# Kernel optimization log

Hardware: AMD Instinct MI355X
Metric: run time of the kernel (lower is better)

Reference implementation:

```python
import jax, jax.numpy as jnp
import numpy as np

N, D_IN, D_OUT = 500000, 128, 128
DROP_P = 0.5


def setup_inputs() -> dict:
    key = jax.random.key(0)
    k1, k2, k3, k4 = jax.random.split(key, 4)
    x = jax.random.normal(k1, (N, D_IN), dtype=jnp.float32)
    weight = jax.random.normal(k2, (D_IN, D_OUT), dtype=jnp.float32)
    support = jax.random.normal(k3, (D_OUT, D_OUT), dtype=jnp.float32)
    # inverted-dropout mask: Bernoulli(keep=1-p) scaled by 1/(1-p), matching F.dropout in training mode
    keep = 1.0 - DROP_P
    u = jax.random.uniform(k4, (N, D_IN), dtype=jnp.float32)
    drop_mask = (u < keep).astype(jnp.float32) / keep
    return {"x": x, "weight": weight, "support": support, "drop_mask": drop_mask}


def reference(x, weight, support, drop_mask):
    # training-mode dropout (deterministic mask), dense transform, right-multiply by support, ReLU
    xd = x * drop_mask                      # [N, D_IN]
    xw = jnp.matmul(xd, weight)             # [N, D_OUT]
    out = jnp.matmul(xw, support)           # [N, D_OUT]
    return jax.nn.relu(out)
```

## Files before the change

kernel.cpp:

```cpp
#include <hip/hip_runtime.h>
#include <hip/hip_bf16.h>


#define D 128

typedef __attribute__((ext_vector_type(8))) short short8;
typedef __attribute__((ext_vector_type(4))) float f32x4;

__device__ __forceinline__ short f2bf(float f) {
    union { __hip_bfloat16 h; short s; } u;
    u.h = __float2bfloat16(f);
    return u.s;
}

__global__ void wprod_kernel(const float* __restrict__ weight,
                             const float* __restrict__ support,
                             unsigned short* __restrict__ wt) {
    __shared__ float wrow[D];
    const int i = blockIdx.x;
    const int j = threadIdx.x;
    wrow[j] = weight[i * D + j];
    __syncthreads();
    float acc = 0.f;
#pragma unroll 8
    for (int k = 0; k < D; ++k)
        acc = fmaf(wrow[k], support[k * D + j], acc);
    union { __hip_bfloat16 h; unsigned short s; } u;
    u.h = __float2bfloat16(acc);
    wt[(size_t)j * D + i] = u.s;
}

__global__ __launch_bounds__(256, 4) void gcn_fused(
    const float* __restrict__ x, const float* __restrict__ mask,
    const unsigned short* __restrict__ wt, float* __restrict__ out,
    int nslabs) {
    __shared__ __align__(16) unsigned short lw[D * D];

    const uint4* src = reinterpret_cast<const uint4*>(wt);
    for (int c = threadIdx.x; c < 2048; c += 256) {
        const int n = c >> 4;
        const int gs = (c & 15) ^ (n & 7);
        *reinterpret_cast<uint4*>(&lw[(n << 7) + (gs << 3)]) = src[c];
    }
    __syncthreads();

    const int lane = threadIdx.x & 63;
    const int m = lane & 15;
    const int quad = lane >> 4;
    const int mx = m & 7;

    const int wave = (int)((blockIdx.x * blockDim.x + threadIdx.x) >> 6);
    const int nwaves = (int)((gridDim.x * blockDim.x) >> 6);

    const int rowoff = m * D + quad * 8;

    int s = wave;
    if (s >= nslabs) return;

    f32x4 vx[8], vm[8];

    {
        const float* xr = x + (size_t)s * (16 * D) + rowoff;
        const float* mr = mask + (size_t)s * (16 * D) + rowoff;
#pragma unroll
        for (int kk = 0; kk < 4; ++kk) {
            vx[2 * kk]     = *reinterpret_cast<const f32x4*>(xr + kk * 32);
            vx[2 * kk + 1] = *reinterpret_cast<const f32x4*>(xr + kk * 32 + 4);
            vm[2 * kk]     = *reinterpret_cast<const f32x4*>(mr + kk * 32);
            vm[2 * kk + 1] = *reinterpret_cast<const f32x4*>(mr + kk * 32 + 4);
        }
    }

    while (true) {
        short8 a[4];
#pragma unroll
        for (int kk = 0; kk < 4; ++kk) {
            f32x4 p0 = vx[2 * kk] * vm[2 * kk];
            f32x4 p1 = vx[2 * kk + 1] * vm[2 * kk + 1];
            short8 v;
            v[0] = f2bf(p0[0]); v[1] = f2bf(p0[1]);
            v[2] = f2bf(p0[2]); v[3] = f2bf(p0[3]);
            v[4] = f2bf(p1[0]); v[5] = f2bf(p1[1]);
            v[6] = f2bf(p1[2]); v[7] = f2bf(p1[3]);
            a[kk] = v;
        }

        const int snext = s + nwaves;
        const bool more = snext < nslabs;
        if (more) {
            const float* xr = x + (size_t)snext * (16 * D) + rowoff;
            const float* mr = mask + (size_t)snext * (16 * D) + rowoff;
#pragma unroll
            for (int kk = 0; kk < 4; ++kk) {
                vx[2 * kk]     = *reinterpret_cast<const f32x4*>(xr + kk * 32);
                vx[2 * kk + 1] = *reinterpret_cast<const f32x4*>(xr + kk * 32 + 4);
                vm[2 * kk]     = *reinterpret_cast<const f32x4*>(mr + kk * 32);
                vm[2 * kk + 1] = *reinterpret_cast<const f32x4*>(mr + kk * 32 + 4);
            }
        }

        float* orow = out + (size_t)s * (16 * D) + m * D;
#pragma unroll
        for (int n = 0; n < 8; ++n) {
            f32x4 acc = {0.f, 0.f, 0.f, 0.f};
#pragma unroll
            for (int kk = 0; kk < 4; ++kk) {
                const short8 b = *reinterpret_cast<const short8*>(
                    &lw[(((n << 4) + m) << 7) + ((((kk << 2) + quad) ^ mx) << 3)]);
                acc = __builtin_amdgcn_mfma_f32_16x16x32_bf16(b, a[kk], acc, 0, 0, 0);
            }
            f32x4 rv;
#pragma unroll
            for (int r = 0; r < 4; ++r) rv[r] = acc[r] > 0.f ? acc[r] : 0.f;
            *reinterpret_cast<f32x4*>(&orow[(n << 4) + (quad << 2)]) = rv;
        }

        if (!more) break;
        s = snext;
    }
}

extern "C" void kernel_launch(void* const* d_in, const int* in_sizes, int n_in,
                              void* d_out, int out_size, void* d_ws, size_t ws_size,
                              hipStream_t stream) {
    const float* x = (const float*)d_in[0];
    const float* weight = (const float*)d_in[1];
    const float* support = (const float*)d_in[2];
    const float* mask = (const float*)d_in[3];
    float* out = (float*)d_out;
    unsigned short* wt = (unsigned short*)d_ws;

    const int nrows = in_sizes[0] / D;
    const int nslabs = nrows / 16;

    wprod_kernel<<<dim3(D), dim3(D), 0, stream>>>(weight, support, wt);
    gcn_fused<<<dim3(1024), dim3(256), 0, stream>>>(x, mask, wt, out, nslabs);
}
```

Measured before the change: 772.1 us.

## Drop register prefetch, use nontemporal loads, double block size for occupancy

```diff
diff --git a/kernel.cpp b/kernel.cpp
--- a/kernel.cpp
+++ b/kernel.cpp
@@ -30,14 +30,14 @@
     wt[(size_t)j * D + i] = u.s;
 }
 
-__global__ __launch_bounds__(256, 4) void gcn_fused(
+__global__ __launch_bounds__(512, 8) void gcn_fused(
     const float* __restrict__ x, const float* __restrict__ mask,
     const unsigned short* __restrict__ wt, float* __restrict__ out,
     int nslabs) {
     __shared__ __align__(16) unsigned short lw[D * D];
 
     const uint4* src = reinterpret_cast<const uint4*>(wt);
-    for (int c = threadIdx.x; c < 2048; c += 256) {
+    for (int c = threadIdx.x; c < 2048; c += 512) {
         const int n = c >> 4;
         const int gs = (c & 15) ^ (n & 7);
         *reinterpret_cast<uint4*>(&lw[(n << 7) + (gs << 3)]) = src[c];
@@ -54,49 +54,29 @@
 
     const int rowoff = m * D + quad * 8;
 
-    int s = wave;
-    if (s >= nslabs) return;
-
-    f32x4 vx[8], vm[8];
-
-    {
+    for (int s = wave; s < nslabs; s += nwaves) {
         const float* xr = x + (size_t)s * (16 * D) + rowoff;
         const float* mr = mask + (size_t)s * (16 * D) + rowoff;
-#pragma unroll
-        for (int kk = 0; kk < 4; ++kk) {
-            vx[2 * kk]     = *reinterpret_cast<const f32x4*>(xr + kk * 32);
-            vx[2 * kk + 1] = *reinterpret_cast<const f32x4*>(xr + kk * 32 + 4);
-            vm[2 * kk]     = *reinterpret_cast<const f32x4*>(mr + kk * 32);
-            vm[2 * kk + 1] = *reinterpret_cast<const f32x4*>(mr + kk * 32 + 4);
-        }
-    }
 
-    while (true) {
         short8 a[4];
 #pragma unroll
         for (int kk = 0; kk < 4; ++kk) {
-            f32x4 p0 = vx[2 * kk] * vm[2 * kk];
-            f32x4 p1 = vx[2 * kk + 1] * vm[2 * kk + 1];
+            f32x4 x0 = __builtin_nontemporal_load(
+                reinterpret_cast<const f32x4*>(xr + kk * 32));
+            f32x4 x1 = __builtin_nontemporal_load(
+                reinterpret_cast<const f32x4*>(xr + kk * 32 + 4));
+            f32x4 m0 = __builtin_nontemporal_load(
+                reinterpret_cast<const f32x4*>(mr + kk * 32));
+            f32x4 m1 = __builtin_nontemporal_load(
+                reinterpret_cast<const f32x4*>(mr + kk * 32 + 4));
+            f32x4 p0 = x0 * m0;
+            f32x4 p1 = x1 * m1;
             short8 v;
             v[0] = f2bf(p0[0]); v[1] = f2bf(p0[1]);
             v[2] = f2bf(p0[2]); v[3] = f2bf(p0[3]);
             v[4] = f2bf(p1[0]); v[5] = f2bf(p1[1]);
             v[6] = f2bf(p1[2]); v[7] = f2bf(p1[3]);
             a[kk] = v;
-        }
-
-        const int snext = s + nwaves;
-        const bool more = snext < nslabs;
-        if (more) {
-            const float* xr = x + (size_t)snext * (16 * D) + rowoff;
-            const float* mr = mask + (size_t)snext * (16 * D) + rowoff;
-#pragma unroll
-            for (int kk = 0; kk < 4; ++kk) {
-                vx[2 * kk]     = *reinterpret_cast<const f32x4*>(xr + kk * 32);
-                vx[2 * kk + 1] = *reinterpret_cast<const f32x4*>(xr + kk * 32 + 4);
-                vm[2 * kk]     = *reinterpret_cast<const f32x4*>(mr + kk * 32);
-                vm[2 * kk + 1] = *reinterpret_cast<const f32x4*>(mr + kk * 32 + 4);
-            }
         }
 
         float* orow = out + (size_t)s * (16 * D) + m * D;
@@ -114,9 +94,6 @@
             for (int r = 0; r < 4; ++r) rv[r] = acc[r] > 0.f ? acc[r] : 0.f;
             *reinterpret_cast<f32x4*>(&orow[(n << 4) + (quad << 2)]) = rv;
         }
-
-        if (!more) break;
-        s = snext;
     }
 }
 
@@ -134,5 +111,5 @@
     const int nslabs = nrows / 16;
 
     wprod_kernel<<<dim3(D), dim3(D), 0, stream>>>(weight, support, wt);
-    gcn_fused<<<dim3(1024), dim3(256), 0, stream>>>(x, mask, wt, out, nslabs);
+    gcn_fused<<<dim3(1024), dim3(512), 0, stream>>>(x, mask, wt, out, nslabs);
 }
```

Result: no change. 764.6 us (-1.0%).
